# Optimization experiments

Hardware: AMD Instinct MI355X
Metric: run time of the kernel (lower is better)

The kernel has to match this reference:

```python
import jax, jax.numpy as jnp
import numpy as np

N_NODES = 10000
N_EDGES = 160000
IN_DIM = 512
HID = 128
OUT = 64


def setup_inputs() -> dict:
    key = jax.random.key(0)
    ks = jax.random.split(key, 8)
    x = jax.random.normal(ks[0], (N_NODES, IN_DIM), dtype=jnp.float32)
    edge_index = jax.random.randint(ks[1], (2, N_EDGES), 0, N_NODES, dtype=jnp.int32)
    s = 0.02
    return {
        "x": x,
        "edge_index": edge_index,
        "W1_l": jax.random.normal(ks[2], (HID, IN_DIM), dtype=jnp.float32) * s,
        "W1_r": jax.random.normal(ks[3], (HID, IN_DIM), dtype=jnp.float32) * s,
        "b1": jnp.zeros((HID,), dtype=jnp.float32),
        "W2_l": jax.random.normal(ks[4], (OUT, HID), dtype=jnp.float32) * s,
        "W2_r": jax.random.normal(ks[5], (OUT, HID), dtype=jnp.float32) * s,
        "b2": jnp.zeros((OUT,), dtype=jnp.float32),
    }


def _sage_conv(x, src, dst, W_l, W_r, b, n_nodes):
    # PyG SAGEConv (aggr='mean', root_weight=True):
    #   out = lin_l(mean over incoming edges of x[src]) + lin_r(x)
    msg = x[src]  # [E, d] gather
    agg = jax.ops.segment_sum(msg, dst, num_segments=n_nodes)  # [N, d]
    cnt = jax.ops.segment_sum(jnp.ones_like(dst, dtype=x.dtype), dst, num_segments=n_nodes)
    agg = agg / jnp.maximum(cnt, 1.0)[:, None]  # mean with empty-node guard
    return agg @ W_l.T + x @ W_r.T + b


def reference(x, edge_index, W1_l, W1_r, b1, W2_l, W2_r, b2):
    src, dst = edge_index[0], edge_index[1]
    n = x.shape[0]
    h = _sage_conv(x, src, dst, W1_l, W1_r, b1, n)
    h = jax.nn.relu(h)
    z = _sage_conv(h, src, dst, W2_l, W2_r, b2, n)
    return z
```

## Files before the change

### kernel.cpp

```cpp
#include <hip/hip_runtime.h>

#define N_NODES 10000
#define N_EDGES 160000
#define IN_DIM 512
#define HID 128
#define OUT_DIM 64
#define CAP 64

typedef __attribute__((ext_vector_type(8))) short bf16x8;
typedef __attribute__((ext_vector_type(4))) float f32x4;

__device__ inline ushort f2b(float f) {
    unsigned u = __float_as_uint(f);
    u += 0x7fff + ((u >> 16) & 1);
    return (ushort)(u >> 16);
}
__device__ inline uint pack2(float a, float b) {
    return (uint)f2b(a) | ((uint)f2b(b) << 16);
}
__device__ inline float blo(uint u) { return __uint_as_float(u << 16); }
__device__ inline float bhi(uint u) { return __uint_as_float(u & 0xffff0000u); }

#define ZCH (N_NODES / 4)
#define W1CH (HID * IN_DIM / 4)
#define W2CH (OUT_DIM * HID / 4)
#define PREP_TOT (ZCH + 2 * W1CH + 2 * W2CH)

__global__ void prep(int* __restrict__ deg,
                     const float* __restrict__ w1l, const float* __restrict__ w1r,
                     const float* __restrict__ w2l, const float* __restrict__ w2r,
                     ushort* __restrict__ wc1, ushort* __restrict__ wc2) {
    int i = blockIdx.x * blockDim.x + threadIdx.x;
    if (i < ZCH) { ((int4*)deg)[i] = make_int4(0, 0, 0, 0); return; }
    i -= ZCH;
    const float* src; ushort* dst;
    if      (i < W1CH)            { src = w1l + (size_t)i * 4;             dst = wc1 + (size_t)i * 4; }
    else if (i < 2 * W1CH)        { int j = i - W1CH;          src = w1r + (size_t)j * 4; dst = wc1 + HID * IN_DIM + (size_t)j * 4; }
    else if (i < 2 * W1CH + W2CH) { int j = i - 2 * W1CH;      src = w2l + (size_t)j * 4; dst = wc2 + (size_t)j * 4; }
    else if (i < PREP_TOT - ZCH)  { int j = i - 2 * W1CH - W2CH; src = w2r + (size_t)j * 4; dst = wc2 + OUT_DIM * HID + (size_t)j * 4; }
    else return;
    float4 v = *reinterpret_cast<const float4*>(src);
    ushort4 o = make_ushort4(f2b(v.x), f2b(v.y), f2b(v.z), f2b(v.w));
    *reinterpret_cast<ushort4*>(dst) = o;
}

template <typename AT, int K, int NT, int HALF>
__device__ __forceinline__ void gemm_body(int bx, int by,
    const AT* __restrict__ A, const ushort* __restrict__ B,
    ushort* __restrict__ C0, float* __restrict__ C1, int M) {
    constexpr int CF = 2;
    __shared__ __align__(16) ushort Asm[32 * 64];
    __shared__ __align__(16) ushort Bsm[64 * 64];

    const int t    = threadIdx.x;
    const int lane = t & 63;
    const int w    = t >> 6;
    const int wr   = w & 1;
    const int wc   = w >> 1;
    const int m0   = by * 32;
    const int n0   = bx * 64;
    const int kch  = lane >> 4;
    const int lrow = lane & 15;

    f32x4 acc[CF] = {};

    for (int k0 = 0; k0 < K; k0 += 64) {
        {
            int row = t >> 3, c = t & 7;
            int m = m0 + row;
            uint4 o = make_uint4(0u, 0u, 0u, 0u);
            if (m < M) {
                if constexpr (sizeof(AT) == 4) {
                    const float* p = (const float*)A + (size_t)m * K + k0 + c * 8;
                    float4 v0 = reinterpret_cast<const float4*>(p)[0];
                    float4 v1 = reinterpret_cast<const float4*>(p)[1];
                    o.x = pack2(v0.x, v0.y); o.y = pack2(v0.z, v0.w);
                    o.z = pack2(v1.x, v1.y); o.w = pack2(v1.z, v1.w);
                } else {
                    o = *reinterpret_cast<const uint4*>((const ushort*)A + (size_t)m * K + k0 + c * 8);
                }
            }
            *reinterpret_cast<uint4*>(&Asm[row * 64 + ((c ^ (row & 7)) << 3)]) = o;
        }
        #pragma unroll
        for (int ch = t; ch < 64 * 8; ch += 256) {
            int row = ch >> 3, c = ch & 7;
            uint4 o = *reinterpret_cast<const uint4*>(&B[(size_t)(n0 + row) * K + k0 + c * 8]);
            *reinterpret_cast<uint4*>(&Bsm[row * 64 + ((c ^ (row & 7)) << 3)]) = o;
        }
        __syncthreads();

        const int arow = wr * 16 + lrow;
        #pragma unroll
        for (int h = 0; h < 2; ++h) {
            int c = h * 4 + kch;
            bf16x8 afr = *reinterpret_cast<const bf16x8*>(&Asm[arow * 64 + ((c ^ (arow & 7)) << 3)]);
            #pragma unroll
            for (int cf = 0; cf < CF; ++cf) {
                int brow = wc * 32 + cf * 16 + lrow;
                bf16x8 bfr = *reinterpret_cast<const bf16x8*>(&Bsm[brow * 64 + ((c ^ (brow & 7)) << 3)]);
                acc[cf] = __builtin_amdgcn_mfma_f32_16x16x32_bf16(afr, bfr, acc[cf], 0, 0, 0);
            }
        }
        __syncthreads();
    }

    #pragma unroll
    for (int cf = 0; cf < CF; ++cf) {
        int col = n0 + wc * 32 + cf * 16 + lrow;
        #pragma unroll
        for (int j = 0; j < 4; ++j) {
            int row = m0 + wr * 16 + kch * 4 + j;
            if (row >= M) continue;
            if (col < HALF) C0[(size_t)row * HALF + col] = f2b(acc[cf][j]);
            else            C1[(size_t)row * (NT - HALF) + (col - HALF)] = acc[cf][j];
        }
    }
}

#define ROWB ((N_NODES + 31) / 32)
#define G1_BLOCKS (4 * ROWB)
#define FILL_BLOCKS ((N_EDGES + 255) / 256)

__global__ __launch_bounds__(256) void fat_gemm1_fill(
    const float* __restrict__ x, const ushort* __restrict__ wc1,
    ushort* __restrict__ XL, float* __restrict__ XR,
    const int* __restrict__ src, const int* __restrict__ dst,
    int* __restrict__ deg, int* __restrict__ bell) {
    int b = blockIdx.x;
    if (b < G1_BLOCKS) {
        gemm_body<float, IN_DIM, 256, HID>(b / ROWB, b % ROWB, x, wc1, XL, XR, N_NODES);
    } else {
        int e = (b - G1_BLOCKS) * 256 + threadIdx.x;
        if (e < N_EDGES) {
            int d = dst[e];
            int pos = atomicAdd(&deg[d], 1);
            if (pos < CAP) bell[d * CAP + pos] = src[e];
        }
    }
}

__global__ __launch_bounds__(256) void gemm2_kernel(
    const ushort* __restrict__ hb, const ushort* __restrict__ wc2,
    ushort* __restrict__ HL, float* __restrict__ HR) {
    gemm_body<ushort, HID, 128, OUT_DIM>(blockIdx.x / ROWB, blockIdx.x % ROWB,
                                         hb, wc2, HL, HR, N_NODES);
}

template <int D, bool RELU, typename OT>
__global__ __launch_bounds__(256) void gather_combine(
    const ushort* __restrict__ V, const float* __restrict__ xr,
    const float* __restrict__ b, const int* __restrict__ deg,
    const int* __restrict__ bell, OT* __restrict__ out) {
    int wave = threadIdx.x >> 6;
    int lane = threadIdx.x & 63;
    int n = blockIdx.x * 4 + wave;
    if (n >= N_NODES) return;

    int d = min(deg[n], CAP);
    const int* lst = bell + (size_t)n * CAP;

    float a0 = 0.f, a1 = 0.f;
    int i = 0;
    if constexpr (D == 128) {
        for (; i + 4 <= d; i += 4) {
            int s0 = lst[i], s1 = lst[i + 1], s2 = lst[i + 2], s3 = lst[i + 3];
            uint u0 = *(const uint*)(V + (size_t)s0 * 128 + lane * 2);
            uint u1 = *(const uint*)(V + (size_t)s1 * 128 + lane * 2);
            uint u2 = *(const uint*)(V + (size_t)s2 * 128 + lane * 2);
            uint u3 = *(const uint*)(V + (size_t)s3 * 128 + lane * 2);
            a0 += blo(u0) + blo(u1) + blo(u2) + blo(u3);
            a1 += bhi(u0) + bhi(u1) + bhi(u2) + bhi(u3);
        }
        for (; i < d; ++i) {
            uint u = *(const uint*)(V + (size_t)lst[i] * 128 + lane * 2);
            a0 += blo(u); a1 += bhi(u);
        }
    } else {
        for (; i + 4 <= d; i += 4) {
            int s0 = lst[i], s1 = lst[i + 1], s2 = lst[i + 2], s3 = lst[i + 3];
            a0 += blo((uint)V[(size_t)s0 * 64 + lane]) + blo((uint)V[(size_t)s1 * 64 + lane])
                + blo((uint)V[(size_t)s2 * 64 + lane]) + blo((uint)V[(size_t)s3 * 64 + lane]);
        }
        for (; i < d; ++i) a0 += blo((uint)V[(size_t)lst[i] * 64 + lane]);
    }

    float inv = (d > 0) ? (1.0f / (float)d) : 0.0f;
    if constexpr (D == 128) {
        float2 xv = *(const float2*)&xr[(size_t)n * 128 + lane * 2];
        float v0 = a0 * inv + xv.x + b[lane * 2];
        float v1 = a1 * inv + xv.y + b[lane * 2 + 1];
        if (RELU) { v0 = fmaxf(v0, 0.f); v1 = fmaxf(v1, 0.f); }
        *(uint*)((ushort*)out + (size_t)n * 128 + lane * 2) = pack2(v0, v1);
    } else {
        float v0 = a0 * inv + xr[(size_t)n * 64 + lane] + b[lane];
        if (RELU) v0 = fmaxf(v0, 0.f);
        ((float*)out)[(size_t)n * 64 + lane] = v0;
    }
}

extern "C" void kernel_launch(void* const* d_in, const int* in_sizes, int n_in,
                              void* d_out, int out_size, void* d_ws, size_t ws_size,
                              hipStream_t stream) {
    const float* x   = (const float*)d_in[0];
    const int*   ei  = (const int*)d_in[1];
    const int*   src = ei;
    const int*   dst = ei + N_EDGES;
    const float* W1l = (const float*)d_in[2];
    const float* W1r = (const float*)d_in[3];
    const float* b1  = (const float*)d_in[4];
    const float* W2l = (const float*)d_in[5];
    const float* W2r = (const float*)d_in[6];
    const float* b2  = (const float*)d_in[7];
    float*       out = (float*)d_out;

    int* deg  = (int*)d_ws;
    int* bell = deg + N_NODES;
    ushort* wc1 = (ushort*)(bell + (size_t)N_NODES * CAP);
    ushort* wc2 = wc1 + (size_t)2 * HID * IN_DIM;
    ushort* XL  = wc2 + (size_t)2 * OUT_DIM * HID;
    float*  XR  = (float*)(XL + (size_t)N_NODES * HID);
    ushort* hb  = (ushort*)(XR + (size_t)N_NODES * HID);
    ushort* HL  = hb + (size_t)N_NODES * HID;
    float*  HR  = (float*)(HL + (size_t)N_NODES * OUT_DIM);

    prep<<<(PREP_TOT + 255) / 256, 256, 0, stream>>>(deg, W1l, W1r, W2l, W2r, wc1, wc2);

    fat_gemm1_fill<<<G1_BLOCKS + FILL_BLOCKS, 256, 0, stream>>>(
        x, wc1, XL, XR, src, dst, deg, bell);

    gather_combine<HID, true, ushort><<<(N_NODES + 3) / 4, 256, 0, stream>>>(
        XL, XR, b1, deg, bell, hb);

    gemm2_kernel<<<2 * ROWB, 256, 0, stream>>>(hb, wc2, HL, HR);

    gather_combine<OUT_DIM, false, float><<<(N_NODES + 3) / 4, 256, 0, stream>>>(
        HL, HR, b2, deg, bell, out);
}
```

Before: 61.95 us.

## Fuse layer-1 gather with layer-2 GEMM and convert weights inline

```diff
diff --git a/kernel.cpp b/kernel.cpp
--- a/kernel.cpp
+++ b/kernel.cpp
@@ -21,34 +21,14 @@
 __device__ inline float blo(uint u) { return __uint_as_float(u << 16); }
 __device__ inline float bhi(uint u) { return __uint_as_float(u & 0xffff0000u); }
 
-#define ZCH (N_NODES / 4)
-#define W1CH (HID * IN_DIM / 4)
-#define W2CH (OUT_DIM * HID / 4)
-#define PREP_TOT (ZCH + 2 * W1CH + 2 * W2CH)
-
-__global__ void prep(int* __restrict__ deg,
-                     const float* __restrict__ w1l, const float* __restrict__ w1r,
-                     const float* __restrict__ w2l, const float* __restrict__ w2r,
-                     ushort* __restrict__ wc1, ushort* __restrict__ wc2) {
+__global__ void zero_deg(int* __restrict__ deg) {
     int i = blockIdx.x * blockDim.x + threadIdx.x;
-    if (i < ZCH) { ((int4*)deg)[i] = make_int4(0, 0, 0, 0); return; }
-    i -= ZCH;
-    const float* src; ushort* dst;
-    if      (i < W1CH)            { src = w1l + (size_t)i * 4;             dst = wc1 + (size_t)i * 4; }
-    else if (i < 2 * W1CH)        { int j = i - W1CH;          src = w1r + (size_t)j * 4; dst = wc1 + HID * IN_DIM + (size_t)j * 4; }
-    else if (i < 2 * W1CH + W2CH) { int j = i - 2 * W1CH;      src = w2l + (size_t)j * 4; dst = wc2 + (size_t)j * 4; }
-    else if (i < PREP_TOT - ZCH)  { int j = i - 2 * W1CH - W2CH; src = w2r + (size_t)j * 4; dst = wc2 + OUT_DIM * HID + (size_t)j * 4; }
-    else return;
-    float4 v = *reinterpret_cast<const float4*>(src);
-    ushort4 o = make_ushort4(f2b(v.x), f2b(v.y), f2b(v.z), f2b(v.w));
-    *reinterpret_cast<ushort4*>(dst) = o;
-}
-
-template <typename AT, int K, int NT, int HALF>
-__device__ __forceinline__ void gemm_body(int bx, int by,
-    const AT* __restrict__ A, const ushort* __restrict__ B,
-    ushort* __restrict__ C0, float* __restrict__ C1, int M) {
-    constexpr int CF = 2;
+    if (i < N_NODES / 4) ((int4*)deg)[i] = make_int4(0, 0, 0, 0);
+}
+
+__device__ __forceinline__ void gemm1_body(int n0, int by,
+    const float* __restrict__ A, const float* __restrict__ bpanel,
+    ushort* __restrict__ XL, float* __restrict__ XR) {
     __shared__ __align__(16) ushort Asm[32 * 64];
     __shared__ __align__(16) ushort Bsm[64 * 64];
 
@@ -58,34 +38,34 @@
     const int wr   = w & 1;
     const int wc   = w >> 1;
     const int m0   = by * 32;
-    const int n0   = bx * 64;
     const int kch  = lane >> 4;
     const int lrow = lane & 15;
 
-    f32x4 acc[CF] = {};
-
-    for (int k0 = 0; k0 < K; k0 += 64) {
+    f32x4 acc[2] = {};
+
+    for (int k0 = 0; k0 < IN_DIM; k0 += 64) {
         {
             int row = t >> 3, c = t & 7;
             int m = m0 + row;
             uint4 o = make_uint4(0u, 0u, 0u, 0u);
-            if (m < M) {
-                if constexpr (sizeof(AT) == 4) {
-                    const float* p = (const float*)A + (size_t)m * K + k0 + c * 8;
-                    float4 v0 = reinterpret_cast<const float4*>(p)[0];
-                    float4 v1 = reinterpret_cast<const float4*>(p)[1];
-                    o.x = pack2(v0.x, v0.y); o.y = pack2(v0.z, v0.w);
-                    o.z = pack2(v1.x, v1.y); o.w = pack2(v1.z, v1.w);
-                } else {
-                    o = *reinterpret_cast<const uint4*>((const ushort*)A + (size_t)m * K + k0 + c * 8);
-                }
+            if (m < N_NODES) {
+                const float* p = A + (size_t)m * IN_DIM + k0 + c * 8;
+                float4 v0 = reinterpret_cast<const float4*>(p)[0];
+                float4 v1 = reinterpret_cast<const float4*>(p)[1];
+                o.x = pack2(v0.x, v0.y); o.y = pack2(v0.z, v0.w);
+                o.z = pack2(v1.x, v1.y); o.w = pack2(v1.z, v1.w);
             }
             *reinterpret_cast<uint4*>(&Asm[row * 64 + ((c ^ (row & 7)) << 3)]) = o;
         }
         #pragma unroll
         for (int ch = t; ch < 64 * 8; ch += 256) {
             int row = ch >> 3, c = ch & 7;
-            uint4 o = *reinterpret_cast<const uint4*>(&B[(size_t)(n0 + row) * K + k0 + c * 8]);
+            const float* p = bpanel + (size_t)row * IN_DIM + k0 + c * 8;
+            float4 v0 = reinterpret_cast<const float4*>(p)[0];
+            float4 v1 = reinterpret_cast<const float4*>(p)[1];
+            uint4 o;
+            o.x = pack2(v0.x, v0.y); o.y = pack2(v0.z, v0.w);
+            o.z = pack2(v1.x, v1.y); o.w = pack2(v1.z, v1.w);
             *reinterpret_cast<uint4*>(&Bsm[row * 64 + ((c ^ (row & 7)) << 3)]) = o;
         }
         __syncthreads();
@@ -96,7 +76,7 @@
             int c = h * 4 + kch;
             bf16x8 afr = *reinterpret_cast<const bf16x8*>(&Asm[arow * 64 + ((c ^ (arow & 7)) << 3)]);
             #pragma unroll
-            for (int cf = 0; cf < CF; ++cf) {
+            for (int cf = 0; cf < 2; ++cf) {
                 int brow = wc * 32 + cf * 16 + lrow;
                 bf16x8 bfr = *reinterpret_cast<const bf16x8*>(&Bsm[brow * 64 + ((c ^ (brow & 7)) << 3)]);
                 acc[cf] = __builtin_amdgcn_mfma_f32_16x16x32_bf16(afr, bfr, acc[cf], 0, 0, 0);
@@ -106,14 +86,14 @@
     }
 
     #pragma unroll
-    for (int cf = 0; cf < CF; ++cf) {
+    for (int cf = 0; cf < 2; ++cf) {
         int col = n0 + wc * 32 + cf * 16 + lrow;
         #pragma unroll
         for (int j = 0; j < 4; ++j) {
             int row = m0 + wr * 16 + kch * 4 + j;
-            if (row >= M) continue;
-            if (col < HALF) C0[(size_t)row * HALF + col] = f2b(acc[cf][j]);
-            else            C1[(size_t)row * (NT - HALF) + (col - HALF)] = acc[cf][j];
+            if (row >= N_NODES) continue;
+            if (col < HID) XL[(size_t)row * HID + col] = f2b(acc[cf][j]);
+            else           XR[(size_t)row * HID + (col - HID)] = acc[cf][j];
         }
     }
 }
@@ -123,13 +103,17 @@
 #define FILL_BLOCKS ((N_EDGES + 255) / 256)
 
 __global__ __launch_bounds__(256) void fat_gemm1_fill(
-    const float* __restrict__ x, const ushort* __restrict__ wc1,
+    const float* __restrict__ x,
+    const float* __restrict__ w1l, const float* __restrict__ w1r,
     ushort* __restrict__ XL, float* __restrict__ XR,
     const int* __restrict__ src, const int* __restrict__ dst,
     int* __restrict__ deg, int* __restrict__ bell) {
     int b = blockIdx.x;
     if (b < G1_BLOCKS) {
-        gemm_body<float, IN_DIM, 256, HID>(b / ROWB, b % ROWB, x, wc1, XL, XR, N_NODES);
+        int bx = b / ROWB, by = b % ROWB;
+        const float* bpanel = (bx < 2) ? (w1l + (size_t)bx * 64 * IN_DIM)
+                                       : (w1r + (size_t)(bx - 2) * 64 * IN_DIM);
+        gemm1_body(bx * 64, by, x, bpanel, XL, XR);
     } else {
         int e = (b - G1_BLOCKS) * 256 + threadIdx.x;
         if (e < N_EDGES) {
@@ -140,18 +124,99 @@
     }
 }
 
-__global__ __launch_bounds__(256) void gemm2_kernel(
-    const ushort* __restrict__ hb, const ushort* __restrict__ wc2,
+__global__ __launch_bounds__(512) void gather1_gemm2(
+    const ushort* __restrict__ XL, const float* __restrict__ XR,
+    const float* __restrict__ b1, const int* __restrict__ deg,
+    const int* __restrict__ bell,
+    const float* __restrict__ w2l, const float* __restrict__ w2r,
     ushort* __restrict__ HL, float* __restrict__ HR) {
-    gemm_body<ushort, HID, 128, OUT_DIM>(blockIdx.x / ROWB, blockIdx.x % ROWB,
-                                         hb, wc2, HL, HR, N_NODES);
-}
-
-template <int D, bool RELU, typename OT>
-__global__ __launch_bounds__(256) void gather_combine(
+    __shared__ __align__(16) ushort Ah[32 * 128];
+    __shared__ __align__(16) ushort Bs[128 * 128];
+
+    const int t    = threadIdx.x;
+    const int lane = t & 63;
+    const int w    = t >> 6;
+    const int base = blockIdx.x * 32;
+
+    #pragma unroll
+    for (int ch = t; ch < 128 * 16; ch += 512) {
+        int row = ch >> 4, c = ch & 15;
+        const float* p = ((row < 64) ? (w2l + (size_t)row * HID)
+                                     : (w2r + (size_t)(row - 64) * HID)) + c * 8;
+        float4 v0 = reinterpret_cast<const float4*>(p)[0];
+        float4 v1 = reinterpret_cast<const float4*>(p)[1];
+        uint4 o;
+        o.x = pack2(v0.x, v0.y); o.y = pack2(v0.z, v0.w);
+        o.z = pack2(v1.x, v1.y); o.w = pack2(v1.z, v1.w);
+        *reinterpret_cast<uint4*>(&Bs[row * 128 + ((c ^ (row & 7)) << 3)]) = o;
+    }
+
+    #pragma unroll
+    for (int q = 0; q < 4; ++q) {
+        int r = w * 4 + q;
+        int n = base + r;
+        float v0 = 0.f, v1 = 0.f;
+        if (n < N_NODES) {
+            int d = min(deg[n], CAP);
+            const int* lst = bell + (size_t)n * CAP;
+            float a0 = 0.f, a1 = 0.f;
+            int i = 0;
+            for (; i + 4 <= d; i += 4) {
+                int s0 = lst[i], s1 = lst[i + 1], s2 = lst[i + 2], s3 = lst[i + 3];
+                uint u0 = *(const uint*)(XL + (size_t)s0 * 128 + lane * 2);
+                uint u1 = *(const uint*)(XL + (size_t)s1 * 128 + lane * 2);
+                uint u2 = *(const uint*)(XL + (size_t)s2 * 128 + lane * 2);
+                uint u3 = *(const uint*)(XL + (size_t)s3 * 128 + lane * 2);
+                a0 += blo(u0) + blo(u1) + blo(u2) + blo(u3);
+                a1 += bhi(u0) + bhi(u1) + bhi(u2) + bhi(u3);
+            }
+            for (; i < d; ++i) {
+                uint u = *(const uint*)(XL + (size_t)lst[i] * 128 + lane * 2);
+                a0 += blo(u); a1 += bhi(u);
+            }
+            float inv = (d > 0) ? (1.0f / (float)d) : 0.0f;
+            float2 xv = *(const float2*)&XR[(size_t)n * 128 + lane * 2];
+            v0 = fmaxf(a0 * inv + xv.x + b1[lane * 2], 0.f);
+            v1 = fmaxf(a1 * inv + xv.y + b1[lane * 2 + 1], 0.f);
+        }
+        int c = lane >> 2;
+        *(uint*)&Ah[r * 128 + ((c ^ (r & 7)) << 3) + (lane & 3) * 2] = pack2(v0, v1);
+    }
+    __syncthreads();
+
+    const int wr = w & 1, cw = w >> 1;
+    const int kch = lane >> 4, lrow = lane & 15;
+    const int arow = wr * 16 + lrow;
+    f32x4 acc[2] = {};
+    #pragma unroll
+    for (int ks = 0; ks < 4; ++ks) {
+        int c = ks * 4 + kch;
+        bf16x8 afr = *reinterpret_cast<const bf16x8*>(&Ah[arow * 128 + ((c ^ (arow & 7)) << 3)]);
+        #pragma unroll
+        for (int cf = 0; cf < 2; ++cf) {
+            int brow = cw * 32 + cf * 16 + lrow;
+            bf16x8 bfr = *reinterpret_cast<const bf16x8*>(&Bs[brow * 128 + ((c ^ (brow & 7)) << 3)]);
+            acc[cf] = __builtin_amdgcn_mfma_f32_16x16x32_bf16(afr, bfr, acc[cf], 0, 0, 0);
+        }
+    }
+
+    #pragma unroll
+    for (int cf = 0; cf < 2; ++cf) {
+        int col = cw * 32 + cf * 16 + lrow;
+        #pragma unroll
+        for (int j = 0; j < 4; ++j) {
+            int row = base + wr * 16 + kch * 4 + j;
+            if (row >= N_NODES) continue;
+            if (col < OUT_DIM) HL[(size_t)row * OUT_DIM + col] = f2b(acc[cf][j]);
+            else               HR[(size_t)row * OUT_DIM + (col - OUT_DIM)] = acc[cf][j];
+        }
+    }
+}
+
+__global__ __launch_bounds__(256) void gather2(
     const ushort* __restrict__ V, const float* __restrict__ xr,
     const float* __restrict__ b, const int* __restrict__ deg,
-    const int* __restrict__ bell, OT* __restrict__ out) {
+    const int* __restrict__ bell, float* __restrict__ out) {
     int wave = threadIdx.x >> 6;
     int lane = threadIdx.x & 63;
     int n = blockIdx.x * 4 + wave;
@@ -160,43 +225,17 @@
     int d = min(deg[n], CAP);
     const int* lst = bell + (size_t)n * CAP;
 
-    float a0 = 0.f, a1 = 0.f;
+    float a0 = 0.f;
     int i = 0;
-    if constexpr (D == 128) {
-        for (; i + 4 <= d; i += 4) {
-            int s0 = lst[i], s1 = lst[i + 1], s2 = lst[i + 2], s3 = lst[i + 3];
-            uint u0 = *(const uint*)(V + (size_t)s0 * 128 + lane * 2);
-            uint u1 = *(const uint*)(V + (size_t)s1 * 128 + lane * 2);
-            uint u2 = *(const uint*)(V + (size_t)s2 * 128 + lane * 2);
-            uint u3 = *(const uint*)(V + (size_t)s3 * 128 + lane * 2);
-            a0 += blo(u0) + blo(u1) + blo(u2) + blo(u3);
-            a1 += bhi(u0) + bhi(u1) + bhi(u2) + bhi(u3);
-        }
-        for (; i < d; ++i) {
-            uint u = *(const uint*)(V + (size_t)lst[i] * 128 + lane * 2);
-            a0 += blo(u); a1 += bhi(u);
-        }
-    } else {
-        for (; i + 4 <= d; i += 4) {
-            int s0 = lst[i], s1 = lst[i + 1], s2 = lst[i + 2], s3 = lst[i + 3];
-            a0 += blo((uint)V[(size_t)s0 * 64 + lane]) + blo((uint)V[(size_t)s1 * 64 + lane])
-                + blo((uint)V[(size_t)s2 * 64 + lane]) + blo((uint)V[(size_t)s3 * 64 + lane]);
-        }
-        for (; i < d; ++i) a0 += blo((uint)V[(size_t)lst[i] * 64 + lane]);
-    }
+    for (; i + 4 <= d; i += 4) {
+        int s0 = lst[i], s1 = lst[i + 1], s2 = lst[i + 2], s3 = lst[i + 3];
+        a0 += blo((uint)V[(size_t)s0 * 64 + lane]) + blo((uint)V[(size_t)s1 * 64 + lane])
+            + blo((uint)V[(size_t)s2 * 64 + lane]) + blo((uint)V[(size_t)s3 * 64 + lane]);
+    }
+    for (; i < d; ++i) a0 += blo((uint)V[(size_t)lst[i] * 64 + lane]);
 
     float inv = (d > 0) ? (1.0f / (float)d) : 0.0f;
-    if constexpr (D == 128) {
-        float2 xv = *(const float2*)&xr[(size_t)n * 128 + lane * 2];
-        float v0 = a0 * inv + xv.x + b[lane * 2];
-        float v1 = a1 * inv + xv.y + b[lane * 2 + 1];
-        if (RELU) { v0 = fmaxf(v0, 0.f); v1 = fmaxf(v1, 0.f); }
-        *(uint*)((ushort*)out + (size_t)n * 128 + lane * 2) = pack2(v0, v1);
-    } else {
-        float v0 = a0 * inv + xr[(size_t)n * 64 + lane] + b[lane];
-        if (RELU) v0 = fmaxf(v0, 0.f);
-        ((float*)out)[(size_t)n * 64 + lane] = v0;
-    }
+    out[(size_t)n * 64 + lane] = a0 * inv + xr[(size_t)n * 64 + lane] + b[lane];
 }
 
 extern "C" void kernel_launch(void* const* d_in, const int* in_sizes, int n_in,
@@ -216,24 +255,17 @@
 
     int* deg  = (int*)d_ws;
     int* bell = deg + N_NODES;
-    ushort* wc1 = (ushort*)(bell + (size_t)N_NODES * CAP);
-    ushort* wc2 = wc1 + (size_t)2 * HID * IN_DIM;
-    ushort* XL  = wc2 + (size_t)2 * OUT_DIM * HID;
-    float*  XR  = (float*)(XL + (size_t)N_NODES * HID);
-    ushort* hb  = (ushort*)(XR + (size_t)N_NODES * HID);
-    ushort* HL  = hb + (size_t)N_NODES * HID;
-    float*  HR  = (float*)(HL + (size_t)N_NODES * OUT_DIM);
-
-    prep<<<(PREP_TOT + 255) / 256, 256, 0, stream>>>(deg, W1l, W1r, W2l, W2r, wc1, wc2);
+    ushort* XL = (ushort*)(bell + (size_t)N_NODES * CAP);
+    float*  XR = (float*)(XL + (size_t)N_NODES * HID);
+    ushort* HL = (ushort*)(XR + (size_t)N_NODES * HID);
+    float*  HR = (float*)(HL + (size_t)N_NODES * OUT_DIM);
+
+    zero_deg<<<(N_NODES / 4 + 255) / 256, 256, 0, stream>>>(deg);
 
     fat_gemm1_fill<<<G1_BLOCKS + FILL_BLOCKS, 256, 0, stream>>>(
-        x, wc1, XL, XR, src, dst, deg, bell);
-
-    gather_combine<HID, true, ushort><<<(N_NODES + 3) / 4, 256, 0, stream>>>(
-        XL, XR, b1, deg, bell, hb);
-
-    gemm2_kernel<<<2 * ROWB, 256, 0, stream>>>(hb, wc2, HL, HR);
-
-    gather_combine<OUT_DIM, false, float><<<(N_NODES + 3) / 4, 256, 0, stream>>>(
-        HL, HR, b2, deg, bell, out);
-}
+        x, W1l, W1r, XL, XR, src, dst, deg, bell);
+
+    gather1_gemm2<<<ROWB, 512, 0, stream>>>(XL, XR, b1, deg, bell, W2l, W2r, HL, HR);
+
+    gather2<<<(N_NODES + 3) / 4, 256, 0, stream>>>(HL, HR, b2, deg, bell, out);
+}
```

Measured after the change: 68.94 us. +11.3%, slower.

## Widen GEMM1 N-tile to 128 and store root-term outputs in bf16

Applied to the files above, without the earlier changes.

```diff
diff --git a/kernel.cpp b/kernel.cpp
--- a/kernel.cpp
+++ b/kernel.cpp
@@ -44,13 +44,13 @@
     *reinterpret_cast<ushort4*>(dst) = o;
 }
 
-template <typename AT, int K, int NT, int HALF>
+template <typename AT, int BN, int K, int NT, int HALF>
 __device__ __forceinline__ void gemm_body(int bx, int by,
     const AT* __restrict__ A, const ushort* __restrict__ B,
-    ushort* __restrict__ C0, float* __restrict__ C1, int M) {
-    constexpr int CF = 2;
+    ushort* __restrict__ C0, ushort* __restrict__ C1, int M) {
+    constexpr int CF = BN / 32;
     __shared__ __align__(16) ushort Asm[32 * 64];
-    __shared__ __align__(16) ushort Bsm[64 * 64];
+    __shared__ __align__(16) ushort Bsm[BN * 64];
 
     const int t    = threadIdx.x;
     const int lane = t & 63;
@@ -58,7 +58,7 @@
     const int wr   = w & 1;
     const int wc   = w >> 1;
     const int m0   = by * 32;
-    const int n0   = bx * 64;
+    const int n0   = bx * BN;
     const int kch  = lane >> 4;
     const int lrow = lane & 15;
 
@@ -83,7 +83,7 @@
             *reinterpret_cast<uint4*>(&Asm[row * 64 + ((c ^ (row & 7)) << 3)]) = o;
         }
         #pragma unroll
-        for (int ch = t; ch < 64 * 8; ch += 256) {
+        for (int ch = t; ch < BN * 8; ch += 256) {
             int row = ch >> 3, c = ch & 7;
             uint4 o = *reinterpret_cast<const uint4*>(&B[(size_t)(n0 + row) * K + k0 + c * 8]);
             *reinterpret_cast<uint4*>(&Bsm[row * 64 + ((c ^ (row & 7)) << 3)]) = o;
@@ -97,7 +97,7 @@
             bf16x8 afr = *reinterpret_cast<const bf16x8*>(&Asm[arow * 64 + ((c ^ (arow & 7)) << 3)]);
             #pragma unroll
             for (int cf = 0; cf < CF; ++cf) {
-                int brow = wc * 32 + cf * 16 + lrow;
+                int brow = wc * (BN / 2) + cf * 16 + lrow;
                 bf16x8 bfr = *reinterpret_cast<const bf16x8*>(&Bsm[brow * 64 + ((c ^ (brow & 7)) << 3)]);
                 acc[cf] = __builtin_amdgcn_mfma_f32_16x16x32_bf16(afr, bfr, acc[cf], 0, 0, 0);
             }
@@ -107,29 +107,29 @@
 
     #pragma unroll
     for (int cf = 0; cf < CF; ++cf) {
-        int col = n0 + wc * 32 + cf * 16 + lrow;
+        int col = n0 + wc * (BN / 2) + cf * 16 + lrow;
         #pragma unroll
         for (int j = 0; j < 4; ++j) {
             int row = m0 + wr * 16 + kch * 4 + j;
             if (row >= M) continue;
             if (col < HALF) C0[(size_t)row * HALF + col] = f2b(acc[cf][j]);
-            else            C1[(size_t)row * (NT - HALF) + (col - HALF)] = acc[cf][j];
+            else            C1[(size_t)row * (NT - HALF) + (col - HALF)] = f2b(acc[cf][j]);
         }
     }
 }
 
 #define ROWB ((N_NODES + 31) / 32)
-#define G1_BLOCKS (4 * ROWB)
+#define G1_BLOCKS (2 * ROWB)
 #define FILL_BLOCKS ((N_EDGES + 255) / 256)
 
 __global__ __launch_bounds__(256) void fat_gemm1_fill(
     const float* __restrict__ x, const ushort* __restrict__ wc1,
-    ushort* __restrict__ XL, float* __restrict__ XR,
+    ushort* __restrict__ XL, ushort* __restrict__ XR,
     const int* __restrict__ src, const int* __restrict__ dst,
     int* __restrict__ deg, int* __restrict__ bell) {
     int b = blockIdx.x;
     if (b < G1_BLOCKS) {
-        gemm_body<float, IN_DIM, 256, HID>(b / ROWB, b % ROWB, x, wc1, XL, XR, N_NODES);
+        gemm_body<float, 128, IN_DIM, 256, HID>(b / ROWB, b % ROWB, x, wc1, XL, XR, N_NODES);
     } else {
         int e = (b - G1_BLOCKS) * 256 + threadIdx.x;
         if (e < N_EDGES) {
@@ -142,16 +142,15 @@
 
 __global__ __launch_bounds__(256) void gemm2_kernel(
     const ushort* __restrict__ hb, const ushort* __restrict__ wc2,
-    ushort* __restrict__ HL, float* __restrict__ HR) {
-    gemm_body<ushort, HID, 128, OUT_DIM>(blockIdx.x / ROWB, blockIdx.x % ROWB,
-                                         hb, wc2, HL, HR, N_NODES);
-}
-
-template <int D, bool RELU, typename OT>
-__global__ __launch_bounds__(256) void gather_combine(
-    const ushort* __restrict__ V, const float* __restrict__ xr,
+    ushort* __restrict__ HL, ushort* __restrict__ HR) {
+    gemm_body<ushort, 64, HID, 128, OUT_DIM>(blockIdx.x / ROWB, blockIdx.x % ROWB,
+                                             hb, wc2, HL, HR, N_NODES);
+}
+
+__global__ __launch_bounds__(256) void gather1(
+    const ushort* __restrict__ V, const ushort* __restrict__ xr,
     const float* __restrict__ b, const int* __restrict__ deg,
-    const int* __restrict__ bell, OT* __restrict__ out) {
+    const int* __restrict__ bell, ushort* __restrict__ out) {
     int wave = threadIdx.x >> 6;
     int lane = threadIdx.x & 63;
     int n = blockIdx.x * 4 + wave;
@@ -162,41 +161,50 @@
 
     float a0 = 0.f, a1 = 0.f;
     int i = 0;
-    if constexpr (D == 128) {
-        for (; i + 4 <= d; i += 4) {
-            int s0 = lst[i], s1 = lst[i + 1], s2 = lst[i + 2], s3 = lst[i + 3];
-            uint u0 = *(const uint*)(V + (size_t)s0 * 128 + lane * 2);
-            uint u1 = *(const uint*)(V + (size_t)s1 * 128 + lane * 2);
-            uint u2 = *(const uint*)(V + (size_t)s2 * 128 + lane * 2);
-            uint u3 = *(const uint*)(V + (size_t)s3 * 128 + lane * 2);
-            a0 += blo(u0) + blo(u1) + blo(u2) + blo(u3);
-            a1 += bhi(u0) + bhi(u1) + bhi(u2) + bhi(u3);
-        }
-        for (; i < d; ++i) {
-            uint u = *(const uint*)(V + (size_t)lst[i] * 128 + lane * 2);
-            a0 += blo(u); a1 += bhi(u);
-        }
-    } else {
-        for (; i + 4 <= d; i += 4) {
-            int s0 = lst[i], s1 = lst[i + 1], s2 = lst[i + 2], s3 = lst[i + 3];
-            a0 += blo((uint)V[(size_t)s0 * 64 + lane]) + blo((uint)V[(size_t)s1 * 64 + lane])
-                + blo((uint)V[(size_t)s2 * 64 + lane]) + blo((uint)V[(size_t)s3 * 64 + lane]);
-        }
-        for (; i < d; ++i) a0 += blo((uint)V[(size_t)lst[i] * 64 + lane]);
+    for (; i + 4 <= d; i += 4) {
+        int s0 = lst[i], s1 = lst[i + 1], s2 = lst[i + 2], s3 = lst[i + 3];
+        uint u0 = *(const uint*)(V + (size_t)s0 * 128 + lane * 2);
+        uint u1 = *(const uint*)(V + (size_t)s1 * 128 + lane * 2);
+        uint u2 = *(const uint*)(V + (size_t)s2 * 128 + lane * 2);
+        uint u3 = *(const uint*)(V + (size_t)s3 * 128 + lane * 2);
+        a0 += blo(u0) + blo(u1) + blo(u2) + blo(u3);
+        a1 += bhi(u0) + bhi(u1) + bhi(u2) + bhi(u3);
+    }
+    for (; i < d; ++i) {
+        uint u = *(const uint*)(V + (size_t)lst[i] * 128 + lane * 2);
+        a0 += blo(u); a1 += bhi(u);
     }
 
     float inv = (d > 0) ? (1.0f / (float)d) : 0.0f;
-    if constexpr (D == 128) {
-        float2 xv = *(const float2*)&xr[(size_t)n * 128 + lane * 2];
-        float v0 = a0 * inv + xv.x + b[lane * 2];
-        float v1 = a1 * inv + xv.y + b[lane * 2 + 1];
-        if (RELU) { v0 = fmaxf(v0, 0.f); v1 = fmaxf(v1, 0.f); }
-        *(uint*)((ushort*)out + (size_t)n * 128 + lane * 2) = pack2(v0, v1);
-    } else {
-        float v0 = a0 * inv + xr[(size_t)n * 64 + lane] + b[lane];
-        if (RELU) v0 = fmaxf(v0, 0.f);
-        ((float*)out)[(size_t)n * 64 + lane] = v0;
-    }
+    uint ux = *(const uint*)(xr + (size_t)n * 128 + lane * 2);
+    float v0 = fmaxf(a0 * inv + blo(ux) + b[lane * 2], 0.f);
+    float v1 = fmaxf(a1 * inv + bhi(ux) + b[lane * 2 + 1], 0.f);
+    *(uint*)(out + (size_t)n * 128 + lane * 2) = pack2(v0, v1);
+}
+
+__global__ __launch_bounds__(256) void gather2(
+    const ushort* __restrict__ V, const ushort* __restrict__ xr,
+    const float* __restrict__ b, const int* __restrict__ deg,
+    const int* __restrict__ bell, float* __restrict__ out) {
+    int wave = threadIdx.x >> 6;
+    int lane = threadIdx.x & 63;
+    int n = blockIdx.x * 4 + wave;
+    if (n >= N_NODES) return;
+
+    int d = min(deg[n], CAP);
+    const int* lst = bell + (size_t)n * CAP;
+
+    float a0 = 0.f;
+    int i = 0;
+    for (; i + 4 <= d; i += 4) {
+        int s0 = lst[i], s1 = lst[i + 1], s2 = lst[i + 2], s3 = lst[i + 3];
+        a0 += blo((uint)V[(size_t)s0 * 64 + lane]) + blo((uint)V[(size_t)s1 * 64 + lane])
+            + blo((uint)V[(size_t)s2 * 64 + lane]) + blo((uint)V[(size_t)s3 * 64 + lane]);
+    }
+    for (; i < d; ++i) a0 += blo((uint)V[(size_t)lst[i] * 64 + lane]);
+
+    float inv = (d > 0) ? (1.0f / (float)d) : 0.0f;
+    out[(size_t)n * 64 + lane] = a0 * inv + blo((uint)xr[(size_t)n * 64 + lane]) + b[lane];
 }
 
 extern "C" void kernel_launch(void* const* d_in, const int* in_sizes, int n_in,
@@ -219,21 +227,19 @@
     ushort* wc1 = (ushort*)(bell + (size_t)N_NODES * CAP);
     ushort* wc2 = wc1 + (size_t)2 * HID * IN_DIM;
     ushort* XL  = wc2 + (size_t)2 * OUT_DIM * HID;
-    float*  XR  = (float*)(XL + (size_t)N_NODES * HID);
-    ushort* hb  = (ushort*)(XR + (size_t)N_NODES * HID);
+    ushort* XR  = XL + (size_t)N_NODES * HID;
+    ushort* hb  = XR + (size_t)N_NODES * HID;
     ushort* HL  = hb + (size_t)N_NODES * HID;
-    float*  HR  = (float*)(HL + (size_t)N_NODES * OUT_DIM);
+    ushort* HR  = HL + (size_t)N_NODES * OUT_DIM;
 
     prep<<<(PREP_TOT + 255) / 256, 256, 0, stream>>>(deg, W1l, W1r, W2l, W2r, wc1, wc2);
 
     fat_gemm1_fill<<<G1_BLOCKS + FILL_BLOCKS, 256, 0, stream>>>(
         x, wc1, XL, XR, src, dst, deg, bell);
 
-    gather_combine<HID, true, ushort><<<(N_NODES + 3) / 4, 256, 0, stream>>>(
-        XL, XR, b1, deg, bell, hb);
+    gather1<<<(N_NODES + 3) / 4, 256, 0, stream>>>(XL, XR, b1, deg, bell, hb);
 
     gemm2_kernel<<<2 * ROWB, 256, 0, stream>>>(hb, wc2, HL, HR);
 
-    gather_combine<OUT_DIM, false, float><<<(N_NODES + 3) / 4, 256, 0, stream>>>(
-        HL, HR, b2, deg, bell, out);
-}
+    gather2<<<(N_NODES + 3) / 4, 256, 0, stream>>>(HL, HR, b2, deg, bell, out);
+}
```

New measurement: 63.23 us. +2.1%, slower.
